# Performance work log

Hardware: AMD Instinct MI355X
Metric: run time of the kernel (lower is better)

Reference implementation:

```python
import jax, jax.numpy as jnp
import numpy as np
from math import sqrt

DK = 64  # head dim from __init__ default


def setup_inputs() -> dict:
    key = jax.random.key(0)
    k1, k2, k3 = jax.random.split(key, 3)
    N, DV = 8192, 64
    Q = jax.random.normal(k1, (N, DK), dtype=jnp.float32)
    K = jax.random.normal(k2, (N, DK), dtype=jnp.float32)
    V = jax.random.normal(k3, (N, DV), dtype=jnp.float32)
    return {"Q": Q, "K": K, "V": V}


def reference(Q, K, V):
    # scores: [Nq, Nk]
    scores = jnp.einsum('qd,kd->qk', Q, K) * (1.0 / sqrt(DK))
    # softmax over key axis (torch nn.Softmax(dim=1) on 2D scores)
    attn = jax.nn.softmax(scores, axis=1)
    return jnp.einsum('qk,kv->qv', attn, V)
```

## Files before the change

### kernel.cpp

```cpp
#include <hip/hip_runtime.h>
#include <math.h>


typedef __bf16 bf16;
typedef __attribute__((ext_vector_type(4)))  __bf16 bf16x4;
typedef __attribute__((ext_vector_type(8)))  __bf16 bf16x8;
typedef __attribute__((ext_vector_type(16))) float  f32x16;

#define DKc 64
#define DVc 64
#define TK  64
#define QW  32
#define NW  4
#define QB  (QW * NW)
#define SCALE_LOG2E 0.1803368801111204f

__device__ __forceinline__ f32x16 mfma_bf16(bf16x8 a, bf16x8 b, f32x16 c) {
    return __builtin_amdgcn_mfma_f32_32x32x16_bf16(a, b, c, 0, 0, 0);
}
__device__ __forceinline__ int rp4(int r) {
    return ((r >> 2) & 1) * 8 + (r & 3) + ((r >> 3) << 2);
}

__global__ __launch_bounds__(256)
void prepass(const float* __restrict__ Q, const float* __restrict__ K,
             const float* __restrict__ V,
             bf16* __restrict__ Qb, bf16* __restrict__ Kb, bf16* __restrict__ Vt,
             int N) {
    const int b = blockIdx.x, tid = threadIdx.x;
    const int nqb = (N * DKc) / (256 * 4);
    if (b < 2 * nqb) {
        bool isQ = b < nqb;
        int idx = (isQ ? b : b - nqb) * 256 + tid;
        float4 v = (isQ ? (const float4*)Q : (const float4*)K)[idx];
        float sc = isQ ? SCALE_LOG2E : 1.0f;
        bf16x4 w;
        w[0] = (bf16)(v.x * sc); w[1] = (bf16)(v.y * sc);
        w[2] = (bf16)(v.z * sc); w[3] = (bf16)(v.w * sc);
        ((bf16x4*)(isQ ? Qb : Kb))[idx] = w;
    } else {
        const int T = b - 2 * nqb;
        __shared__ float sT[64][65];
#pragma unroll
        for (int p = 0; p < 4; ++p) {
            int fi = p * 256 + tid;
            int e0 = fi * 4;
            int key = e0 >> 6, dv = e0 & 63;
            float4 v = ((const float4*)(V + (size_t)T * 64 * DVc))[fi];
            sT[dv + 0][key] = v.x; sT[dv + 1][key] = v.y;
            sT[dv + 2][key] = v.z; sT[dv + 3][key] = v.w;
        }
        __syncthreads();
#pragma unroll
        for (int w = 0; w < 2; ++w) {
            int vidx = w * 256 + tid;
            int dv = vidx >> 3, j0 = (vidx & 7) * 8;
            bf16x8 o;
#pragma unroll
            for (int i = 0; i < 8; ++i) {
                int j = j0 + i;
                int ks = (j & 48) | rp4(j & 15);
                o[i] = (bf16)sT[dv][ks];
            }
            *(bf16x8*)(Vt + (size_t)dv * N + T * 64 + j0) = o;
        }
    }
}

__global__ __launch_bounds__(256, 4)
void attn_fwd_mfma(const bf16* __restrict__ Qb, const bf16* __restrict__ Kb,
                   const bf16* __restrict__ Vt,
                   float* __restrict__ Opart, float* __restrict__ Mpart,
                   float* __restrict__ Lpart, float* __restrict__ Out,
                   int N, int splits, int chunk) {
    __shared__ __align__(16) short sK[TK * DKc];
    __shared__ __align__(16) short sV[DVc * TK];

    const int tid  = threadIdx.x;
    const int wid  = tid >> 6;
    const int lane = tid & 63;
    const int l31  = lane & 31;
    const int h    = lane >> 5;

    const int qbase = blockIdx.x * QB + wid * QW;
    const int q     = qbase + l31;
    const int sp    = blockIdx.y;

    bf16x8 qf[4];
#pragma unroll
    for (int f = 0; f < 4; ++f)
        qf[f] = *(const bf16x8*)(Qb + (size_t)q * DKc + f * 16 + h * 8);

    f32x16 O0 = {0}, O1 = {0};
    float m = -1e30f, lsum = 0.f;

    const int k0 = sp * chunk;
    int k1 = k0 + chunk; if (k1 > N) k1 = N;

    const char* KbB = (const char*)Kb;
    const char* VtB = (const char*)Vt;
    char* sKc = (char*)sK;
    char* sVc = (char*)sV;
    const size_t vrow = (size_t)N * 2;

    for (int t0 = k0; t0 < k1; t0 += TK) {
        __syncthreads();
#pragma unroll
        for (int p = 0; p < 2; ++p) {
            int o   = p * 4096 + wid * 1024 + lane * 16;
            int key = o >> 7;
            int so  = o ^ ((key & 7) << 4);
            __builtin_amdgcn_global_load_lds(
                (const __attribute__((address_space(1))) void*)(KbB + (size_t)t0 * 128 + so),
                (__attribute__((address_space(3))) void*)(sKc + p * 4096 + wid * 1024),
                16, 0, 0);
        }
#pragma unroll
        for (int p = 0; p < 2; ++p) {
            int o  = p * 4096 + wid * 1024 + lane * 16;
            int dv = o >> 7;
            int kb = o & 127;
            int so = kb ^ ((dv & 7) << 4);
            __builtin_amdgcn_global_load_lds(
                (const __attribute__((address_space(1))) void*)(VtB + (size_t)dv * vrow + (size_t)t0 * 2 + so),
                (__attribute__((address_space(3))) void*)(sVc + p * 4096 + wid * 1024),
                16, 0, 0);
        }
        __syncthreads();

        f32x16 d0 = {0}, d1 = {0};
#pragma unroll
        for (int f = 0; f < 4; ++f) {
            int keyA = l31, keyB = 32 + l31;
            int ba = ((keyA * 128) + f * 32 + h * 16) ^ ((keyA & 7) << 4);
            int bb = ((keyB * 128) + f * 32 + h * 16) ^ ((keyB & 7) << 4);
            bf16x8 kf0 = *(const bf16x8*)(sKc + ba);
            bf16x8 kf1 = *(const bf16x8*)(sKc + bb);
            d0 = mfma_bf16(kf0, qf[f], d0);
            d1 = mfma_bf16(kf1, qf[f], d1);
        }

        float tm = -1e30f;
#pragma unroll
        for (int r = 0; r < 16; ++r) tm = fmaxf(tm, fmaxf(d0[r], d1[r]));
        tm = fmaxf(tm, __shfl_xor(tm, 32));

        float fs = 1.f;
        if (__any(tm > m + 10.f)) {
            float mn = fmaxf(m, tm);
            fs = __builtin_amdgcn_exp2f(m - mn);
            m = mn;
#pragma unroll
            for (int r = 0; r < 16; ++r) {
                int qr = (r & 3) + 8 * (r >> 2) + 4 * h;
                float fr = __shfl(fs, (lane & 32) | qr);
                O0[r] *= fr; O1[r] *= fr;
            }
        }

        float psum = 0.f;
#pragma unroll
        for (int r = 0; r < 16; ++r) {
            d0[r] = __builtin_amdgcn_exp2f(d0[r] - m); psum += d0[r];
            d1[r] = __builtin_amdgcn_exp2f(d1[r] - m); psum += d1[r];
        }
        psum += __shfl_xor(psum, 32);
        lsum = lsum * fs + psum;

        bf16x8 pa[4];
#pragma unroll
        for (int j = 0; j < 8; ++j) {
            pa[0][j] = (bf16)d0[j];
            pa[1][j] = (bf16)d0[8 + j];
            pa[2][j] = (bf16)d1[j];
            pa[3][j] = (bf16)d1[8 + j];
        }

#pragma unroll
        for (int kb = 0; kb < 4; ++kb) {
            int dvA = l31, dvB = 32 + l31;
            int ba = ((dvA * 128) + kb * 32 + h * 16) ^ ((dvA & 7) << 4);
            int bb = ((dvB * 128) + kb * 32 + h * 16) ^ ((dvB & 7) << 4);
            bf16x8 vf0 = *(const bf16x8*)(sVc + ba);
            bf16x8 vf1 = *(const bf16x8*)(sVc + bb);
            O0 = mfma_bf16(pa[kb], vf0, O0);
            O1 = mfma_bf16(pa[kb], vf1, O1);
        }
    }

    if (splits == 1) {
        float inv = 1.f / lsum;
#pragma unroll
        for (int r = 0; r < 16; ++r) {
            int qr = (r & 3) + 8 * (r >> 2) + 4 * h;
            float fr = __shfl(inv, (lane & 32) | qr);
            int qq = qbase + qr;
            Out[(size_t)qq * DVc + l31]      = O0[r] * fr;
            Out[(size_t)qq * DVc + 32 + l31] = O1[r] * fr;
        }
    } else {
#pragma unroll
        for (int r = 0; r < 16; ++r) {
            int qr = (r & 3) + 8 * (r >> 2) + 4 * h;
            int qq = qbase + qr;
            size_t off = ((size_t)sp * N + qq) * DVc;
            Opart[off + l31]      = O0[r];
            Opart[off + 32 + l31] = O1[r];
        }
        if (lane < 32) {
            Mpart[(size_t)sp * N + q] = m;
            Lpart[(size_t)sp * N + q] = lsum;
        }
    }
}

__global__ __launch_bounds__(256)
void attn_combine(const float* __restrict__ Opart, const float* __restrict__ Mpart,
                  const float* __restrict__ Lpart, float* __restrict__ Out,
                  int N, int splits) {
    const int t  = blockIdx.x * blockDim.x + threadIdx.x;
    const int q  = t >> 4;
    const int d4 = t & 15;

    float M = -1e30f;
    for (int s = 0; s < splits; ++s) M = fmaxf(M, Mpart[(size_t)s * N + q]);

    float4 acc = make_float4(0.f, 0.f, 0.f, 0.f);
    float  L = 0.f;
    for (int s = 0; s < splits; ++s) {
        float w = __builtin_amdgcn_exp2f(Mpart[(size_t)s * N + q] - M);
        L += w * Lpart[(size_t)s * N + q];
        float4 ov = *(const float4*)(Opart + ((size_t)s * N + q) * DVc + d4 * 4);
        acc.x += w * ov.x; acc.y += w * ov.y; acc.z += w * ov.z; acc.w += w * ov.w;
    }
    float inv = 1.f / L;
    *(float4*)(Out + (size_t)q * DVc + d4 * 4) =
        make_float4(acc.x * inv, acc.y * inv, acc.z * inv, acc.w * inv);
}

extern "C" void kernel_launch(void* const* d_in, const int* in_sizes, int n_in,
                              void* d_out, int out_size, void* d_ws, size_t ws_size,
                              hipStream_t stream) {
    const float* Q = (const float*)d_in[0];
    const float* K = (const float*)d_in[1];
    const float* V = (const float*)d_in[2];
    float* Out = (float*)d_out;

    const int N = in_sizes[0] / DKc;

    const size_t bfbytes = (size_t)N * DKc * sizeof(short);
    bf16* Qb = (bf16*)d_ws;
    bf16* Kb = (bf16*)((char*)d_ws + bfbytes);
    bf16* Vt = (bf16*)((char*)d_ws + 2 * bfbytes);
    char* rest = (char*)d_ws + 3 * bfbytes;
    size_t rest_sz = (ws_size > 3 * bfbytes) ? ws_size - 3 * bfbytes : 0;

    int splits = 16;
    while (splits > 1 &&
           (size_t)splits * (size_t)N * (DVc + 2) * sizeof(float) > rest_sz)
        splits >>= 1;
    int chunk = (N + splits - 1) / splits;
    chunk = ((chunk + TK - 1) / TK) * TK;

    float* Opart = (float*)rest;
    float* Mpart = Opart + (size_t)splits * N * DVc;
    float* Lpart = Mpart + (size_t)splits * N;

    const int nqb = (N * DKc) / (256 * 4);
    prepass<<<2 * nqb + N / TK, 256, 0, stream>>>(Q, K, V, Qb, Kb, Vt, N);

    dim3 grid(N / QB, splits);
    attn_fwd_mfma<<<grid, 256, 0, stream>>>(Qb, Kb, Vt, Opart, Mpart, Lpart, Out,
                                            N, splits, chunk);
    if (splits > 1) {
        int total = N * 16;
        attn_combine<<<total / 256, 256, 0, stream>>>(Opart, Mpart, Lpart, Out,
                                                      N, splits);
    }
}
```

Baseline: 100.6 us.

## Double-buffer K/V LDS tiles to overlap global loads with MFMA compute

Splits the K and V shared-memory tiles into two buffers. The next tile is issued with async global-to-LDS loads while the current tile is being computed, and explicit vmcnt waits plus s_barrier replace the __syncthreads pair. The aim is to hide global memory latency behind the QK and PV MFMAs. In exchange, LDS use doubles (32KB per block), which may cut occupancy under the 4-block launch bound. The hand-written waitcnt also assumes exactly 4 outstanding loads per tile, and the tile count uses integer division, which assumes the chunk is a multiple of TK.

```diff
diff --git a/kernel.cpp b/kernel.cpp
--- a/kernel.cpp
+++ b/kernel.cpp
@@ -73,8 +73,8 @@
                    float* __restrict__ Opart, float* __restrict__ Mpart,
                    float* __restrict__ Lpart, float* __restrict__ Out,
                    int N, int splits, int chunk) {
-    __shared__ __align__(16) short sK[TK * DKc];
-    __shared__ __align__(16) short sV[DVc * TK];
+    __shared__ __align__(16) short sK[2][TK * DKc];
+    __shared__ __align__(16) short sV[2][DVc * TK];
 
     const int tid  = threadIdx.x;
     const int wid  = tid >> 6;
@@ -96,15 +96,15 @@
 
     const int k0 = sp * chunk;
     int k1 = k0 + chunk; if (k1 > N) k1 = N;
+    const int ntiles = (k1 - k0) / TK;
 
     const char* KbB = (const char*)Kb;
     const char* VtB = (const char*)Vt;
-    char* sKc = (char*)sK;
-    char* sVc = (char*)sV;
     const size_t vrow = (size_t)N * 2;
 
-    for (int t0 = k0; t0 < k1; t0 += TK) {
-        __syncthreads();
+    auto stage = [&](int buf, int t0) {
+        char* sKb = (char*)&sK[buf][0];
+        char* sVb = (char*)&sV[buf][0];
 #pragma unroll
         for (int p = 0; p < 2; ++p) {
             int o   = p * 4096 + wid * 1024 + lane * 16;
@@ -112,7 +112,7 @@
             int so  = o ^ ((key & 7) << 4);
             __builtin_amdgcn_global_load_lds(
                 (const __attribute__((address_space(1))) void*)(KbB + (size_t)t0 * 128 + so),
-                (__attribute__((address_space(3))) void*)(sKc + p * 4096 + wid * 1024),
+                (__attribute__((address_space(3))) void*)(sKb + p * 4096 + wid * 1024),
                 16, 0, 0);
         }
 #pragma unroll
@@ -123,10 +123,26 @@
             int so = kb ^ ((dv & 7) << 4);
             __builtin_amdgcn_global_load_lds(
                 (const __attribute__((address_space(1))) void*)(VtB + (size_t)dv * vrow + (size_t)t0 * 2 + so),
-                (__attribute__((address_space(3))) void*)(sVc + p * 4096 + wid * 1024),
+                (__attribute__((address_space(3))) void*)(sVb + p * 4096 + wid * 1024),
                 16, 0, 0);
         }
-        __syncthreads();
+    };
+
+    stage(0, k0);
+    int cur = 0;
+
+    for (int it = 0; it < ntiles; ++it) {
+        if (it + 1 < ntiles) {
+            stage(cur ^ 1, k0 + (it + 1) * TK);
+            asm volatile("s_waitcnt vmcnt(4)" ::: "memory");
+        } else {
+            asm volatile("s_waitcnt vmcnt(0)" ::: "memory");
+        }
+        __builtin_amdgcn_sched_barrier(0);
+        __builtin_amdgcn_s_barrier();
+
+        const char* sKc = (const char*)&sK[cur][0];
+        const char* sVc = (const char*)&sV[cur][0];
 
         f32x16 d0 = {0}, d1 = {0};
 #pragma unroll
@@ -186,6 +202,9 @@
             O0 = mfma_bf16(pa[kb], vf0, O0);
             O1 = mfma_bf16(pa[kb], vf1, O1);
         }
+
+        __builtin_amdgcn_s_barrier();
+        cur ^= 1;
     }
 
     if (splits == 1) {
```

New measurement: 100.2 us. No clear change (-0.3%).
